# Performance work log

Measured on AMD Instinct MI355X. Metric: run time of the kernel, lower is better.

## Reference

```python
import jax, jax.numpy as jnp
import numpy as np
from jax import lax

QMAX = 15.0   # 4-bit unsigned activation levels
BN_EPS = 1e-5


def _binarize_irnet(w):
    # IR-Net style 1-bit weights: per-output-channel normalize, sign, rescale by mean |w|.
    mu = jnp.mean(w, axis=(1, 2, 3), keepdims=True)
    std = jnp.std(w, axis=(1, 2, 3), keepdims=True)
    wn = (w - mu) / (std + 1e-5)
    scale = jnp.mean(jnp.abs(wn), axis=(1, 2, 3), keepdims=True)
    wc = jnp.clip(wn, -1.0, 1.0)
    # STE: forward=sign(wn), backward=hardtanh passthrough
    bw = wc + lax.stop_gradient(jnp.sign(wn) - wc)
    return bw * scale


def _lsq_act_4bit(x, alpha):
    # LSQ unsigned 4-bit: clamp(x/alpha, 0, 15), round with STE, rescale.
    xs = jnp.clip(x / alpha, 0.0, QMAX)
    xq = xs + lax.stop_gradient(jnp.round(xs) - xs)
    return xq * alpha


def _qconv_bn_relu(x, w, alpha, g, b, m, v, stride):
    xq = _lsq_act_4bit(x, alpha)
    bw = _binarize_irnet(w)
    y = lax.conv_general_dilated(
        xq, bw, window_strides=(stride, stride), padding=((1, 1), (1, 1)),
        dimension_numbers=('NCHW', 'OIHW', 'NCHW'))
    inv = g / jnp.sqrt(v + BN_EPS)
    y = y * inv[None, :, None, None] + (b - m * inv)[None, :, None, None]
    return jax.nn.relu(y)


def setup_inputs() -> dict:
    key = jax.random.key(0)
    ks = jax.random.split(key, 3)
    B, C, H, W = 32, 256, 56, 56
    x = jax.random.normal(ks[0], (B, C, H, W), dtype=jnp.float32)
    w1 = jax.random.normal(ks[1], (C, C, 3, 3), dtype=jnp.float32) * 0.05
    w2 = jax.random.normal(ks[2], (C, C, 3, 3), dtype=jnp.float32) * 0.05
    ones = jnp.ones((C,), jnp.float32)
    zeros = jnp.zeros((C,), jnp.float32)
    return {
        'x': x,
        'w1': w1, 'alpha1': jnp.float32(0.1), 'g1': ones, 'b1': zeros, 'm1': zeros, 'v1': ones,
        'w2': w2, 'alpha2': jnp.float32(0.1), 'g2': ones, 'b2': zeros, 'm2': zeros, 'v2': ones,
    }


def reference(x, w1, alpha1, g1, b1, m1, v1, w2, alpha2, g2, b2, m2, v2):
    stride = 1
    h = _qconv_bn_relu(x, w1, alpha1, g1, b1, m1, v1, stride)
    out = _qconv_bn_relu(h, w2, alpha2, g2, b2, m2, v2, 1)
    return out
```

## Files before the change

### kernel.cpp

```cpp
#include <hip/hip_runtime.h>
#include <math.h>

typedef int v4i __attribute__((ext_vector_type(4)));
typedef int v16i __attribute__((ext_vector_type(16)));
typedef unsigned long long u64;

#define Bn 32
#define Cc 256
#define Hh 56
#define Ww 56
#define RSTR (34 * 256)
#define ACT_LDS (6 * RSTR)
#define NSTG (6 * 34 * 16)

__device__ __forceinline__ float block_sum(float v, float* red) {
#pragma unroll
    for (int off = 32; off > 0; off >>= 1) v += __shfl_down(v, off, 64);
    const int wv = threadIdx.x >> 6;
    __syncthreads();
    if ((threadIdx.x & 63) == 0) red[wv] = v;
    __syncthreads();
    return red[0] + red[1] + red[2] + red[3];
}

__global__ __launch_bounds__(256) void k_binpack(const float* __restrict__ w,
                                                 signed char* __restrict__ wf,
                                                 float* __restrict__ wsc) {
    __shared__ float red[4];
    const int o = blockIdx.x;
    const float* wo = w + (size_t)o * 2304;
    const int t = threadIdx.x;
    float v[9];
    float s = 0.f, s2 = 0.f;
#pragma unroll
    for (int i = 0; i < 9; ++i) {
        v[i] = wo[t * 9 + i];
        s += v[i];
        s2 += v[i] * v[i];
    }
    s = block_sum(s, red);
    s2 = block_sum(s2, red);
    const float mu = s * (1.f / 2304.f);
    const float sd = sqrtf(fmaxf(s2 * (1.f / 2304.f) - mu * mu, 0.f));
    float sa = 0.f;
#pragma unroll
    for (int i = 0; i < 9; ++i) sa += fabsf(v[i] - mu);
    sa = block_sum(sa, red);
    if (t == 0) wsc[o] = (sa * (1.f / 2304.f)) / (sd + 1e-5f);
    const int c = t, c32 = c >> 5, hf = (c >> 4) & 1, j = c & 15;
    const int lane = (hf << 5) | (o & 31), octile = o >> 5;
#pragma unroll
    for (int tap = 0; tap < 9; ++tap) {
        const float d = v[tap] - mu;
        const signed char sg = (d > 0.f) ? 1 : ((d < 0.f) ? -1 : 0);
        wf[(size_t)(((tap * 8 + c32) * 8 + octile) * 64 + lane) * 16 + j] = sg;
    }
}

__global__ void k_prep(const float* __restrict__ g1, const float* __restrict__ b1,
                       const float* __restrict__ m1, const float* __restrict__ v1,
                       const float* __restrict__ g2, const float* __restrict__ b2,
                       const float* __restrict__ m2, const float* __restrict__ v2,
                       const float* __restrict__ a1p, const float* __restrict__ a2p,
                       const float* __restrict__ ws1, const float* __restrict__ ws2,
                       float* __restrict__ ep) {
    const int i = threadIdx.x;
    const float i1 = g1[i] / sqrtf(v1[i] + 1e-5f);
    const float i2 = g2[i] / sqrtf(v2[i] + 1e-5f);
    ep[i] = a1p[0] * ws1[i] * i1;
    ep[256 + i] = b1[i] - m1[i] * i1;
    ep[512 + i] = a2p[0] * ws2[i] * i2;
    ep[768 + i] = b2[i] - m2[i] * i2;
}

__global__ __launch_bounds__(256) void k_quant_nhwc(const float* __restrict__ x,
                                                    unsigned char* __restrict__ xq,
                                                    const float* __restrict__ ap) {
    __shared__ unsigned char q[3584];
    const int bid = blockIdx.x;
    const int cg = bid & 3;
    const int h = (bid >> 2) % Hh;
    const int n = bid / (4 * Hh);
    const float a = ap[0];
    const int c0 = cg * 64;
    for (int i = threadIdx.x; i < 3584; i += 256) {
        const int cl = i / 56;
        const int w = i - cl * 56;
        const float v = x[(((size_t)n * Cc + c0 + cl) * Hh + h) * Ww + w];
        const float xs = fminf(fmaxf(v / a, 0.f), 15.f);
        q[w * 64 + (((cl >> 2) ^ (w & 15)) << 2) + (cl & 3)] = (unsigned char)(int)rintf(xs);
    }
    __syncthreads();
    const unsigned int* q32 = (const unsigned int*)q;
    unsigned int* dst = (unsigned int*)xq + ((size_t)(n * Hh + h) * Ww) * 32;
    for (int j = threadIdx.x; j < 448; j += 256) {
        const int w = j >> 3, g8l = (j >> 1) & 3, hf = j & 1;
        const unsigned int lo = q32[w * 16 + ((g8l * 4 + hf) ^ (w & 15))];
        const unsigned int hi = q32[w * 16 + ((g8l * 4 + 2 + hf) ^ (w & 15))];
        dst[w * 32 + (cg * 4 + g8l) * 2 + hf] = lo | (hi << 4);
    }
}

template <bool QOUT>
__global__ __launch_bounds__(256, 3) void k_conv(const unsigned char* __restrict__ xin,
                                                 const signed char* __restrict__ wf,
                                                 const float* __restrict__ ep,
                                                 const float* __restrict__ a2p,
                                                 unsigned char* __restrict__ hq,
                                                 float* __restrict__ yout) {
    __shared__ __align__(16) unsigned char sm[ACT_LDS];
    const int bid = blockIdx.x;
    const int oh = bid & 1;
    const int mh = (bid >> 1) & 1;
    const int hb = (bid >> 2) % 14;
    const int n = (bid >> 2) / 14;
    const int h0 = hb * 4;
    const int mbase = mh * 32;
    const int tid = threadIdx.x;
    const int boff = bid & 7;

    {
        u64 tmp[13];
#pragma unroll
        for (int k = 0; k < 13; ++k) {
            int u = tid + (k << 8);
            u = u > (NSTG - 1) ? (NSTG - 1) : u;
            const int r = u / 544;
            const int rem = u - r * 544;
            const int col = rem >> 4;
            const int t8 = rem & 15;
            int y = h0 - 1 + r;
            int xi = mbase - 1 + col;
            y = y < 0 ? 0 : (y > 55 ? 55 : y);
            xi = xi < 0 ? 0 : (xi > 55 ? 55 : xi);
            tmp[k] = *(const u64*)(xin + ((((size_t)n * Hh + y) * Ww + xi) << 7) + (t8 << 3));
        }
#pragma unroll
        for (int k = 0; k < 13; ++k) {
            const int u = tid + (k << 8);
            if (u < NSTG) {
                const int r = u / 544;
                const int rem = u - r * 544;
                const int col = rem >> 4;
                const int t8 = rem & 15;
                const int y = h0 - 1 + r;
                const int xi = mbase - 1 + col;
                const u64 p = ((unsigned)y < 56u && (unsigned)xi < 56u) ? tmp[k] : 0;
                const u64 lo = p & 0x0F0F0F0F0F0F0F0FULL;
                const u64 hi = (p >> 4) & 0x0F0F0F0F0F0F0F0FULL;
                v4i wv;
                wv[0] = (int)lo;
                wv[1] = (int)(lo >> 32);
                wv[2] = (int)hi;
                wv[3] = (int)(hi >> 32);
                *(v4i*)(sm + r * RSTR + col * 256 + ((t8 ^ (col & 15)) << 4)) = wv;
            }
        }
    }
    __syncthreads();

    const int lane = tid & 63;
    const int g = tid >> 6;
    const int half = lane >> 5;
    const int lm = lane & 31;
    const int octile = oh * 4 + g;

    v16i acc[4] = {};
    const v4i* wpg = (const v4i*)wf + octile * 64 + lane;

    int pkw[3];
#pragma unroll
    for (int kw = 0; kw < 3; ++kw) {
        const int col = lm + kw;
        pkw[kw] = (col * 256) ^ (half << 4) ^ ((col & 15) << 4);
    }

#pragma unroll 1
    for (int ii = 0; ii < 8; ++ii) {
        const int c32 = (ii + boff) & 7;
        v4i aw[9];
#pragma unroll
        for (int tap = 0; tap < 9; ++tap) aw[tap] = wpg[(tap * 8 + c32) << 9];
        const int cs = c32 << 5;
#pragma unroll
        for (int kw = 0; kw < 3; ++kw) {
            const unsigned char* bp = sm + (pkw[kw] ^ cs);
            v4i bfr[6];
#pragma unroll
            for (int ar = 0; ar < 6; ++ar)
                bfr[ar] = *(const v4i*)(bp + ar * RSTR);
#pragma unroll
            for (int kh = 0; kh < 3; ++kh) {
#pragma unroll
                for (int r = 0; r < 4; ++r)
                    acc[r] = __builtin_amdgcn_mfma_i32_32x32x32_i8(aw[kh * 3 + kw],
                                                                   bfr[r + kh], acc[r], 0, 0, 0);
            }
        }
    }

    if constexpr (QOUT) {
        __syncthreads();
        unsigned int* hb = (unsigned int*)sm;
        const float inva = 1.0f / a2p[0];
        const int oc0w = oh * 128 + g * 32;
        const int d0 = 4 * g + half;
#pragma unroll
        for (int r = 0; r < 4; ++r) {
            const v16i av = acc[r];
            unsigned int pk0 = 0, pk1 = 0;
#pragma unroll
            for (int q = 0; q < 4; ++q) {
                const int oc = oc0w + 4 * half + q;
                const unsigned int c0 = (unsigned int)(int)rintf(
                    fminf(fmaxf(fmaf((float)av[q], ep[oc], ep[256 + oc]), 0.f) * inva, 15.f));
                const unsigned int c1 = (unsigned int)(int)rintf(
                    fminf(fmaxf(fmaf((float)av[4 + q], ep[oc + 8], ep[264 + oc]), 0.f) * inva, 15.f));
                const unsigned int c2 = (unsigned int)(int)rintf(
                    fminf(fmaxf(fmaf((float)av[8 + q], ep[oc + 16], ep[272 + oc]), 0.f) * inva, 15.f));
                const unsigned int c3 = (unsigned int)(int)rintf(
                    fminf(fmaxf(fmaf((float)av[12 + q], ep[oc + 24], ep[280 + oc]), 0.f) * inva, 15.f));
                pk0 |= (c0 | (c1 << 4)) << (8 * q);
                pk1 |= (c2 | (c3 << 4)) << (8 * q);
            }
            const int rb = (r * 32 + lm) * 16;
            hb[rb + (d0 ^ (lm & 15))] = pk0;
            hb[rb + ((d0 + 2) ^ (lm & 15))] = pk1;
        }
        __syncthreads();
        unsigned int* dst = (unsigned int*)hq;
        for (int j = tid; j < 4 * 32 * 16; j += 256) {
            const int rw = j >> 4, dw = j & 15;
            const int r = rw >> 5, wl = rw & 31;
            const int w = mbase + wl;
            if (w < 56)
                dst[((size_t)((n * Hh + h0 + r) * Ww) + w) * 32 + oh * 16 + dw] =
                    hb[(rw << 4) + (dw ^ (wl & 15))];
        }
    } else {
        const int w = mbase + lm;
        if (w < 56) {
            float* dst = yout + (size_t)n * Cc * 3136 + (size_t)h0 * 56 + w;
#pragma unroll
            for (int r = 0; r < 4; ++r) {
                const v16i av = acc[r];
#pragma unroll
                for (int reg = 0; reg < 16; ++reg) {
                    const int oc = oh * 128 + g * 32 + (reg & 3) + 8 * (reg >> 2) + 4 * half;
                    dst[(size_t)oc * 3136 + r * 56] =
                        fmaxf(fmaf((float)av[reg], ep[oc], ep[256 + oc]), 0.f);
                }
            }
        }
    }
}

extern "C" void kernel_launch(void* const* d_in, const int* in_sizes, int n_in,
                              void* d_out, int out_size, void* d_ws, size_t ws_size,
                              hipStream_t stream) {
    const float* x = (const float*)d_in[0];
    const float* w1 = (const float*)d_in[1];
    const float* a1 = (const float*)d_in[2];
    const float* g1 = (const float*)d_in[3];
    const float* b1 = (const float*)d_in[4];
    const float* m1 = (const float*)d_in[5];
    const float* v1 = (const float*)d_in[6];
    const float* w2 = (const float*)d_in[7];
    const float* a2 = (const float*)d_in[8];
    const float* g2 = (const float*)d_in[9];
    const float* b2 = (const float*)d_in[10];
    const float* m2 = (const float*)d_in[11];
    const float* v2 = (const float*)d_in[12];

    signed char* wf1 = (signed char*)d_ws;
    signed char* wf2 = wf1 + 589824;
    float* wsc1 = (float*)(wf2 + 589824);
    float* wsc2 = wsc1 + 256;
    float* ep = wsc2 + 256;
    unsigned char* xq1 = (unsigned char*)(ep + 1024);
    unsigned char* hq = xq1 + (size_t)12845056;

    k_binpack<<<256, 256, 0, stream>>>(w1, wf1, wsc1);
    k_binpack<<<256, 256, 0, stream>>>(w2, wf2, wsc2);
    k_prep<<<1, 256, 0, stream>>>(g1, b1, m1, v1, g2, b2, m2, v2, a1, a2, wsc1, wsc2, ep);
    k_quant_nhwc<<<Bn * Hh * 4, 256, 0, stream>>>(x, xq1, a1);

    k_conv<true><<<1792, 256, 0, stream>>>(xq1, wf1, ep, a2, hq, nullptr);
    k_conv<false><<<1792, 256, 0, stream>>>(hq, wf2, ep + 512, nullptr, nullptr, (float*)d_out);
}
```

Baseline: 179.4 us.

## Stream conv weights into LDS via double-buffered global_load_lds pipeline

Replaces per-iteration register loads of nine weight fragments with asynchronous global-to-LDS DMA into a two-slot buffer. Each phase prefetches the next kw-column's three taps while MFMAs run on the current one, with raised wave priority around the MFMA block. The channel-group rotation offset now also varies per wave. The added 24 KB of LDS lowers the occupancy target from three blocks per CU to two, and the last phase issues a prefetch past the loop end.

New measurement: 183.6 us. 2.3% more time.

```diff
diff --git a/kernel.cpp b/kernel.cpp
--- a/kernel.cpp
+++ b/kernel.cpp
@@ -11,6 +11,7 @@
 #define Ww 56
 #define RSTR (34 * 256)
 #define ACT_LDS (6 * RSTR)
+#define ABUF_LDS 24576
 #define NSTG (6 * 34 * 16)
 
 __device__ __forceinline__ float block_sum(float v, float* red) {
@@ -101,14 +102,51 @@
     }
 }
 
+#define DMA(SLOT, KW, II)                                                      \
+    do {                                                                       \
+        const int c32d_ = ((II) + boff) & 7;                                   \
+        _Pragma("unroll") for (int kh_ = 0; kh_ < 3; ++kh_) {                  \
+            const int fi_ = ((kh_ * 3 + (KW)) * 8 + c32d_) * 8 + octile;       \
+            __builtin_amdgcn_global_load_lds(                                  \
+                (const __attribute__((address_space(1))) void*)(wf +           \
+                    ((size_t)fi_ << 10) + (lane << 4)),                        \
+                (__attribute__((address_space(3))) void*)(abuf +               \
+                    (SLOT)*12288 + (g * 3 + kh_) * 1024),                      \
+                16, 0, 0);                                                     \
+        }                                                                      \
+    } while (0)
+
+#define PHASE(SLOT, KW, II, NSLOT, NKW, NII)                                   \
+    do {                                                                       \
+        DMA(NSLOT, NKW, NII);                                                  \
+        asm volatile("s_waitcnt vmcnt(3)" ::: "memory");                       \
+        __builtin_amdgcn_sched_barrier(0);                                     \
+        v4i aw_[3];                                                            \
+        _Pragma("unroll") for (int kh_ = 0; kh_ < 3; ++kh_)                    \
+            aw_[kh_] = *(const v4i*)(abuf + (SLOT)*12288 +                     \
+                                     (g * 3 + kh_) * 1024 + (lane << 4));      \
+        const int c32_ = ((II) + boff) & 7;                                    \
+        const unsigned char* bp_ = sm + (pkw[(KW)] ^ (c32_ << 5));             \
+        v4i bfr_[6];                                                           \
+        _Pragma("unroll") for (int ar_ = 0; ar_ < 6; ++ar_)                    \
+            bfr_[ar_] = *(const v4i*)(bp_ + ar_ * RSTR);                       \
+        __builtin_amdgcn_s_setprio(1);                                         \
+        _Pragma("unroll") for (int kh_ = 0; kh_ < 3; ++kh_)                    \
+            _Pragma("unroll") for (int r_ = 0; r_ < 4; ++r_)                   \
+                acc[r_] = __builtin_amdgcn_mfma_i32_32x32x32_i8(               \
+                    aw_[kh_], bfr_[r_ + kh_], acc[r_], 0, 0, 0);               \
+        __builtin_amdgcn_s_setprio(0);                                         \
+    } while (0)
+
 template <bool QOUT>
-__global__ __launch_bounds__(256, 3) void k_conv(const unsigned char* __restrict__ xin,
+__global__ __launch_bounds__(256, 2) void k_conv(const unsigned char* __restrict__ xin,
                                                  const signed char* __restrict__ wf,
                                                  const float* __restrict__ ep,
                                                  const float* __restrict__ a2p,
                                                  unsigned char* __restrict__ hq,
                                                  float* __restrict__ yout) {
-    __shared__ __align__(16) unsigned char sm[ACT_LDS];
+    __shared__ __align__(16) unsigned char sm[ACT_LDS + ABUF_LDS];
+    unsigned char* abuf = sm + ACT_LDS;
     const int bid = blockIdx.x;
     const int oh = bid & 1;
     const int mh = (bid >> 1) & 1;
@@ -117,7 +155,6 @@
     const int h0 = hb * 4;
     const int mbase = mh * 32;
     const int tid = threadIdx.x;
-    const int boff = bid & 7;
 
     {
         u64 tmp[13];
@@ -164,9 +201,9 @@
     const int half = lane >> 5;
     const int lm = lane & 31;
     const int octile = oh * 4 + g;
+    const int boff = ((bid << 2) | g) & 7;
 
     v16i acc[4] = {};
-    const v4i* wpg = (const v4i*)wf + octile * 64 + lane;
 
     int pkw[3];
 #pragma unroll
@@ -175,28 +212,17 @@
         pkw[kw] = (col * 256) ^ (half << 4) ^ ((col & 15) << 4);
     }
 
+    DMA(0, 0, 0);
+
 #pragma unroll 1
-    for (int ii = 0; ii < 8; ++ii) {
-        const int c32 = (ii + boff) & 7;
-        v4i aw[9];
-#pragma unroll
-        for (int tap = 0; tap < 9; ++tap) aw[tap] = wpg[(tap * 8 + c32) << 9];
-        const int cs = c32 << 5;
-#pragma unroll
-        for (int kw = 0; kw < 3; ++kw) {
-            const unsigned char* bp = sm + (pkw[kw] ^ cs);
-            v4i bfr[6];
-#pragma unroll
-            for (int ar = 0; ar < 6; ++ar)
-                bfr[ar] = *(const v4i*)(bp + ar * RSTR);
-#pragma unroll
-            for (int kh = 0; kh < 3; ++kh) {
-#pragma unroll
-                for (int r = 0; r < 4; ++r)
-                    acc[r] = __builtin_amdgcn_mfma_i32_32x32x32_i8(aw[kh * 3 + kw],
-                                                                   bfr[r + kh], acc[r], 0, 0, 0);
-            }
-        }
+    for (int s6 = 0; s6 < 4; ++s6) {
+        const int ii = s6 * 2;
+        PHASE(0, 0, ii,     1, 1, ii);
+        PHASE(1, 1, ii,     0, 2, ii);
+        PHASE(0, 2, ii,     1, 0, ii + 1);
+        PHASE(1, 0, ii + 1, 0, 1, ii + 1);
+        PHASE(0, 1, ii + 1, 1, 2, ii + 1);
+        PHASE(1, 2, ii + 1, 0, 0, ii + 2);
     }
 
     if constexpr (QOUT) {
```
